# Performance work log

Hardware: AMD Instinct MI355X
Metric: run time of the kernel (lower is better)

The kernel has to match this reference:

```python
import jax, jax.numpy as jnp
import numpy as np

N = 10000      # num_nodes
RP = 16        # latent relations
E = 64         # emb_dim
R = 8000       # num triples (MLP input dim)
NT = 8000      # unique (s,o) pairs (unique by construction)
LW = 64        # lwidth
C = 16         # num_classes
NREL = 50      # num_rels (<= R columns actually used in nhots)


def setup_inputs() -> dict:
    rng = np.random.default_rng(0)
    # unique (s,o) pairs -> nt == R, deterministic shapes
    pair_ids = rng.choice(N * N, size=R, replace=False)
    s = (pair_ids // N).astype(np.int32)
    o = (pair_ids % N).astype(np.int32)
    p = rng.integers(0, NREL, size=R)
    nhots = np.zeros((NT, R), np.float32)
    nhots[np.arange(NT), p] = 1.0
    # replicate index construction from __init__ exactly
    rm = np.arange(RP, dtype=np.int32)[:, None]           # (RP,1)
    s_exp = np.broadcast_to(s[None, :], (RP, NT)).reshape(-1)
    o_exp = np.broadcast_to(o[None, :], (RP, NT)).reshape(-1)
    se = (s[None, :] * rm).reshape(-1)
    oe = (o[None, :] * rm).reshape(-1)
    hindices = np.stack([s_exp, oe], axis=1).astype(np.int32)  # into (N, N*RP)
    vindices = np.stack([se, o_exp], axis=1).astype(np.int32)  # into (N*RP, N)

    key = jax.random.key(0)
    ks = jax.random.split(key, 6)
    inv = lambda d: 1.0 / np.sqrt(d)
    return {
        'nhots': jnp.asarray(nhots),
        'w1a': jax.random.normal(ks[0], (R, LW), jnp.float32) * inv(R),
        'b1a': jnp.zeros((LW,), jnp.float32),
        'w1b': jax.random.normal(ks[1], (LW, RP), jnp.float32) * inv(LW),
        'b1b': jnp.zeros((RP,), jnp.float32),
        'w2a': jax.random.normal(ks[2], (R, LW), jnp.float32) * inv(R),
        'b2a': jnp.zeros((LW,), jnp.float32),
        'w2b': jax.random.normal(ks[3], (LW, RP), jnp.float32) * inv(LW),
        'b2b': jnp.zeros((RP,), jnp.float32),
        'weights1': jax.random.normal(ks[4], (RP, N, E), jnp.float32) * 0.02,
        'bias1': jnp.zeros((E,), jnp.float32),
        'weights2': jax.random.normal(ks[5], (RP, E, C), jnp.float32) * 0.02,
        'bias2': jnp.zeros((C,), jnp.float32),
        'hindices': jnp.asarray(hindices),
        'vindices': jnp.asarray(vindices),
    }


def _latents(nhots, wa, ba, wb, bb):
    # Linear -> ReLU -> Linear -> softmax over rp, then .t().reshape(-1)
    lat = jax.nn.softmax(jax.nn.relu(nhots @ wa + ba) @ wb + bb, axis=1)  # (NT, RP)
    return lat.T.reshape(-1)  # (RP*NT,) — rm-major, matching index construction


def reference(nhots, w1a, b1a, w1b, b1b, w2a, b2a, w2b, b2b,
              weights1, bias1, weights2, bias2, hindices, vindices):
    hrow, hcol = hindices[:, 0], hindices[:, 1]
    vrow, vcol = vindices[:, 0], vindices[:, 1]

    # --- layer 1: A1 (N, N*RP), column-normalized ---
    lat1 = _latents(nhots, w1a, b1a, w1b, b1b)
    colsum = jax.ops.segment_sum(lat1, hcol, num_segments=N * RP)
    lat1 = lat1 / colsum[hcol]
    Xw = weights1.reshape(RP * N, E)
    h = jax.ops.segment_sum(lat1[:, None] * Xw[hcol], hrow, num_segments=N)  # (N, E)
    h = jax.nn.relu(h + bias1)

    # --- layer 2: A2 (N*RP, N), row-normalized ---
    lat2 = _latents(nhots, w2a, b2a, w2b, b2b)
    rowsum = jax.ops.segment_sum(lat2, vrow, num_segments=N * RP)
    lat2 = lat2 / rowsum[vrow]
    h2 = jax.ops.segment_sum(lat2[:, None] * h[vcol], vrow, num_segments=N * RP)
    h2 = h2.reshape(RP, N, E)

    out = jnp.einsum('rhc,rnh->nc', weights2, h2) + bias2  # (N, C)
    return out
```

## Files before the change

### kernel.cpp

```cpp
#include <hip/hip_runtime.h>
#include <hip/hip_bf16.h>


#define N_     10000
#define RP_    16
#define E_     64
#define R_     8000
#define NT_    8000
#define C_     16
#define NE_    128000
#define BK_    32

#define WS_ZERO_UNITS 330080

__global__ void k_lat(const float* __restrict__ nhots,
                      const float* __restrict__ w1a, const float* __restrict__ b1a,
                      const float* __restrict__ w1b, const float* __restrict__ b1b,
                      const float* __restrict__ w2a, const float* __restrict__ b2a,
                      const float* __restrict__ w2b, const float* __restrict__ b2b,
                      const int* __restrict__ hind, const int* __restrict__ vind,
                      float* __restrict__ lat1t, float* __restrict__ lat2,
                      float* __restrict__ colsum, float* __restrict__ rowsum,
                      int* __restrict__ cnt, int* __restrict__ order2,
                      float* __restrict__ out, const float* __restrict__ bias2) {
    __shared__ float zb[4][128];
    __shared__ float r0[2];
    const int lane = threadIdx.x & 63;
    const int wv   = threadIdx.x >> 6;
    const int t    = blockIdx.x * 4 + wv;

    if (threadIdx.x < 80) {
        const int i = blockIdx.x * 80 + threadIdx.x;
        out[i] = bias2[i & 15];
    }

    const float4 v = reinterpret_cast<const float4*>(nhots + (size_t)t * R_)[lane];
    float acc1 = 0.f, acc2 = 0.f;
    const float comp[4] = {v.x, v.y, v.z, v.w};
    #pragma unroll
    for (int c = 0; c < 4; ++c) {
        unsigned long long m = __ballot(comp[c] != 0.0f);
        while (m) {
            const int src = __ffsll(m) - 1;
            m &= m - 1;
            const float val = __shfl(comp[c], src);
            const int col = src * 4 + c;
            acc1 += val * w1a[col * 64 + lane];
            acc2 += val * w2a[col * 64 + lane];
        }
    }
    if (threadIdx.x == 0) { r0[0] = 0.f; r0[1] = 0.f; }
    zb[wv][lane]      = fmaxf(acc1 + b1a[lane], 0.f);
    zb[wv][64 + lane] = fmaxf(acc2 + b2a[lane], 0.f);
    __syncthreads();

    const int g = lane >> 4, r = lane & 15;
    float pre = 0.f;
    if (g < 2) {
        const float* wb = (g == 0) ? w1b : w2b;
        pre = ((g == 0) ? b1b : b2b)[r];
        const float* z = &zb[wv][g * 64];
        #pragma unroll
        for (int l = 0; l < 64; ++l) pre += z[l] * wb[l * 16 + r];
    }
    float mx = pre;
    #pragma unroll
    for (int m = 8; m >= 1; m >>= 1) mx = fmaxf(mx, __shfl_xor(mx, m, 16));
    const float e = expf(pre - mx);
    float s = e;
    #pragma unroll
    for (int m = 8; m >= 1; m >>= 1) s += __shfl_xor(s, m, 16);
    const float lt = e / s;

    const int s_t = hind[2 * t];
    const int o_t = vind[2 * t + 1];
    if (g == 0) {
        lat1t[t * 16 + r] = lt;
        if (r) atomicAdd(colsum + o_t * r, lt);
        else   atomicAdd(&r0[0], lt);
    } else if (g == 1) {
        lat2[r * NT_ + t] = lt;
        if (r) atomicAdd(rowsum + s_t * r, lt);
        else   atomicAdd(&r0[1], lt);
    } else if (g == 2 && r == 0) {
        const int pos = atomicAdd(cnt + s_t, 1);
        order2[s_t * BK_ + pos] = t | (o_t << 13);
    }
    __syncthreads();
    if (threadIdx.x == 0) atomicAdd(colsum, r0[0]);
    if (threadIdx.x == 1) atomicAdd(rowsum, r0[1]);
}

__global__ void k_hg(const float* __restrict__ lat1t, const float* __restrict__ colsum,
                     const int* __restrict__ cnt, const int* __restrict__ order2,
                     const float* __restrict__ w1,
                     const float* __restrict__ bias1, float* __restrict__ hbuf) {
    const int lane = threadIdx.x & 63;
    const int n = blockIdx.x * 4 + (threadIdx.x >> 6);
    const int m = cnt[n];
    float acc = 0.f;
    for (int j = 0; j < m; ++j) {
        const int e = order2[n * BK_ + j];
        const int t   = e & 8191;
        const int o_t = e >> 13;
        float ln = 0.f;
        if (lane < 16) ln = lat1t[t * 16 + lane] / colsum[o_t * lane];
        #pragma unroll
        for (int r = 0; r < 16; ++r) {
            const float a = __shfl(ln, r);
            acc += a * w1[(o_t * r) * 64 + lane];
        }
    }
    hbuf[n * 64 + lane] = fmaxf(acc + bias1[lane], 0.f);
}

__global__ void k_h2all(const float* __restrict__ lat2, const float* __restrict__ rowsum,
                        const int* __restrict__ vind, const float* __restrict__ hbuf,
                        const float* __restrict__ w2, float* __restrict__ out,
                        float* __restrict__ h2r0, int* __restrict__ done) {
    const int lane = threadIdx.x & 63;
    const int wv   = threadIdx.x >> 6;

    if (blockIdx.x >= 512) {
        __shared__ int is_last;
        const int wg = (blockIdx.x - 512) * 4 + wv;
        float acc = 0.f;
        for (int t = wg; t < NT_; t += 256) {
            const int vc = vind[2 * t + 1];
            acc += lat2[t] * hbuf[vc * 64 + lane];
        }
        acc /= rowsum[0];
        atomicAdd(&h2r0[lane], acc);
        __threadfence();
        __syncthreads();
        if (threadIdx.x == 0) is_last = (atomicAdd(done, 1) == 63);
        __syncthreads();
        if (is_last) {
            __threadfence();
            if (threadIdx.x < 16) {
                const int c = threadIdx.x;
                float acc2 = 0.f;
                #pragma unroll
                for (int hh = 0; hh < 64; ++hh) acc2 += w2[hh * 16 + c] * h2r0[hh];
                atomicAdd(&out[c], acc2);
            }
        }
        return;
    }

    __shared__ float sw2[16384];
    for (int i = threadIdx.x; i < 16384; i += 256) sw2[i] = w2[i];
    __syncthreads();

    const int c = lane & 15;
    const int quarter = lane >> 4;
    for (int e = blockIdx.x * 4 + wv; e < 120000; e += 512 * 4) {
        const int k  = NT_ + e;
        const int q  = vind[2 * k];
        const int vc = vind[2 * k + 1];
        const float val = lat2[k] / rowsum[q];
        const int rp = q / N_;
        const int np = q - rp * N_;
        const float u = val * hbuf[vc * 64 + lane];
        float partial = 0.f;
        #pragma unroll
        for (int j = 0; j < 16; ++j) {
            const int hh = quarter * 16 + ((j + quarter) & 15);
            const float hv = __shfl(u, hh);
            partial += hv * sw2[rp * 1024 + hh * 16 + c];
        }
        partial += __shfl_xor(partial, 16);
        partial += __shfl_xor(partial, 32);
        if (quarter == 0) atomicAdd(&out[np * 16 + c], partial);
    }
}

extern "C" void kernel_launch(void* const* d_in, const int* in_sizes, int n_in,
                              void* d_out, int out_size, void* d_ws, size_t ws_size,
                              hipStream_t stream) {
    const float* nhots    = (const float*)d_in[0];
    const float* w1a      = (const float*)d_in[1];
    const float* b1a      = (const float*)d_in[2];
    const float* w1b      = (const float*)d_in[3];
    const float* b1b      = (const float*)d_in[4];
    const float* w2a      = (const float*)d_in[5];
    const float* b2a      = (const float*)d_in[6];
    const float* w2b      = (const float*)d_in[7];
    const float* b2b      = (const float*)d_in[8];
    const float* weights1 = (const float*)d_in[9];
    const float* bias1    = (const float*)d_in[10];
    const float* weights2 = (const float*)d_in[11];
    const float* bias2    = (const float*)d_in[12];
    const int*   hind     = (const int*)d_in[13];
    const int*   vind     = (const int*)d_in[14];
    float* out = (float*)d_out;

    float* ws     = (float*)d_ws;
    float* colsum = ws;
    float* rowsum = ws + 160000;
    float* h2r0   = ws + 320000;
    int*   cnt    = (int*)(ws + 320064);
    int*   done   = (int*)(ws + 330064);
    int*   order2 = (int*)(ws + 330080);
    float* hbuf   = ws + 650080;
    float* lat1t  = ws + 1290080;
    float* lat2   = ws + 1418080;

    hipMemsetAsync(d_ws, 0, WS_ZERO_UNITS * sizeof(float), stream);
    k_lat<<<2000, 256, 0, stream>>>(nhots, w1a, b1a, w1b, b1b, w2a, b2a, w2b, b2b,
                                    hind, vind, lat1t, lat2, colsum, rowsum, cnt,
                                    order2, out, bias2);
    k_hg<<<2500, 256, 0, stream>>>(lat1t, colsum, cnt, order2, weights1, bias1, hbuf);
    k_h2all<<<576, 256, 0, stream>>>(lat2, rowsum, vind, hbuf, weights2, out, h2r0, done);
}
```

Baseline: 454.9 us.

## Precompute h·W2 per node and replace scatter atomics with bucketed gather

```diff
diff --git a/kernel.cpp b/kernel.cpp
--- a/kernel.cpp
+++ b/kernel.cpp
@@ -8,10 +8,10 @@
 #define R_     8000
 #define NT_    8000
 #define C_     16
-#define NE_    128000
 #define BK_    32
-
-#define WS_ZERO_UNITS 330080
+#define BK2_   96
+
+#define WS_ZERO_UNITS 340000
 
 __global__ void k_lat(const float* __restrict__ nhots,
                       const float* __restrict__ w1a, const float* __restrict__ b1a,
@@ -22,17 +22,12 @@
                       float* __restrict__ lat1t, float* __restrict__ lat2,
                       float* __restrict__ colsum, float* __restrict__ rowsum,
                       int* __restrict__ cnt, int* __restrict__ order2,
-                      float* __restrict__ out, const float* __restrict__ bias2) {
+                      int* __restrict__ cnt2, int* __restrict__ bucket2) {
     __shared__ float zb[4][128];
     __shared__ float r0[2];
     const int lane = threadIdx.x & 63;
     const int wv   = threadIdx.x >> 6;
     const int t    = blockIdx.x * 4 + wv;
-
-    if (threadIdx.x < 80) {
-        const int i = blockIdx.x * 80 + threadIdx.x;
-        out[i] = bias2[i & 15];
-    }
 
     const float4 v = reinterpret_cast<const float4*>(nhots + (size_t)t * R_)[lane];
     float acc1 = 0.f, acc2 = 0.f;
@@ -82,96 +77,121 @@
         lat2[r * NT_ + t] = lt;
         if (r) atomicAdd(rowsum + s_t * r, lt);
         else   atomicAdd(&r0[1], lt);
-    } else if (g == 2 && r == 0) {
-        const int pos = atomicAdd(cnt + s_t, 1);
-        order2[s_t * BK_ + pos] = t | (o_t << 13);
+    } else if (g == 2) {
+        if (r == 0) {
+            const int pos = atomicAdd(cnt + s_t, 1);
+            order2[s_t * BK_ + pos] = t | (o_t << 13);
+        } else {
+            const int q = s_t * r;
+            const int rp = q / N_;
+            const int np = q - rp * N_;
+            const int pos = atomicAdd(cnt2 + np, 1);
+            bucket2[np * BK2_ + pos] = t | (r << 13) | (rp << 17);
+        }
     }
     __syncthreads();
     if (threadIdx.x == 0) atomicAdd(colsum, r0[0]);
     if (threadIdx.x == 1) atomicAdd(rowsum, r0[1]);
 }
 
-__global__ void k_hg(const float* __restrict__ lat1t, const float* __restrict__ colsum,
-                     const int* __restrict__ cnt, const int* __restrict__ order2,
-                     const float* __restrict__ w1,
-                     const float* __restrict__ bias1, float* __restrict__ hbuf) {
-    const int lane = threadIdx.x & 63;
-    const int n = blockIdx.x * 4 + (threadIdx.x >> 6);
-    const int m = cnt[n];
-    float acc = 0.f;
-    for (int j = 0; j < m; ++j) {
-        const int e = order2[n * BK_ + j];
-        const int t   = e & 8191;
-        const int o_t = e >> 13;
-        float ln = 0.f;
-        if (lane < 16) ln = lat1t[t * 16 + lane] / colsum[o_t * lane];
-        #pragma unroll
-        for (int r = 0; r < 16; ++r) {
-            const float a = __shfl(ln, r);
-            acc += a * w1[(o_t * r) * 64 + lane];
-        }
-    }
-    hbuf[n * 64 + lane] = fmaxf(acc + bias1[lane], 0.f);
-}
-
-__global__ void k_h2all(const float* __restrict__ lat2, const float* __restrict__ rowsum,
-                        const int* __restrict__ vind, const float* __restrict__ hbuf,
-                        const float* __restrict__ w2, float* __restrict__ out,
-                        float* __restrict__ h2r0, int* __restrict__ done) {
+__global__ void k_hgg(const float* __restrict__ lat1t, const float* __restrict__ colsum,
+                      const int* __restrict__ cnt, const int* __restrict__ order2,
+                      const float* __restrict__ w1, const float* __restrict__ bias1,
+                      const float* __restrict__ w2, float* __restrict__ g,
+                      float* __restrict__ out) {
+    __shared__ float sw2[16384];
     const int lane = threadIdx.x & 63;
     const int wv   = threadIdx.x >> 6;
-
-    if (blockIdx.x >= 512) {
-        __shared__ int is_last;
-        const int wg = (blockIdx.x - 512) * 4 + wv;
-        float acc = 0.f;
-        for (int t = wg; t < NT_; t += 256) {
-            const int vc = vind[2 * t + 1];
-            acc += lat2[t] * hbuf[vc * 64 + lane];
-        }
-        acc /= rowsum[0];
-        atomicAdd(&h2r0[lane], acc);
-        __threadfence();
-        __syncthreads();
-        if (threadIdx.x == 0) is_last = (atomicAdd(done, 1) == 63);
-        __syncthreads();
-        if (is_last) {
-            __threadfence();
-            if (threadIdx.x < 16) {
-                const int c = threadIdx.x;
-                float acc2 = 0.f;
-                #pragma unroll
-                for (int hh = 0; hh < 64; ++hh) acc2 += w2[hh * 16 + c] * h2r0[hh];
-                atomicAdd(&out[c], acc2);
-            }
-        }
-        return;
-    }
-
-    __shared__ float sw2[16384];
+    if (blockIdx.x == 0 && threadIdx.x < 16) out[threadIdx.x] = 0.f;
     for (int i = threadIdx.x; i < 16384; i += 256) sw2[i] = w2[i];
     __syncthreads();
 
-    const int c = lane & 15;
-    const int quarter = lane >> 4;
-    for (int e = blockIdx.x * 4 + wv; e < 120000; e += 512 * 4) {
-        const int k  = NT_ + e;
-        const int q  = vind[2 * k];
-        const int vc = vind[2 * k + 1];
-        const float val = lat2[k] / rowsum[q];
-        const int rp = q / N_;
-        const int np = q - rp * N_;
-        const float u = val * hbuf[vc * 64 + lane];
-        float partial = 0.f;
-        #pragma unroll
-        for (int j = 0; j < 16; ++j) {
-            const int hh = quarter * 16 + ((j + quarter) & 15);
-            const float hv = __shfl(u, hh);
-            partial += hv * sw2[rp * 1024 + hh * 16 + c];
-        }
-        partial += __shfl_xor(partial, 16);
-        partial += __shfl_xor(partial, 32);
-        if (quarter == 0) atomicAdd(&out[np * 16 + c], partial);
+    const int q = lane >> 4, c = lane & 15;
+    const int nbase = blockIdx.x * 32 + wv * 8;
+    float u[8];
+    #pragma unroll 1
+    for (int i = 0; i < 8; ++i) {
+        const int n = nbase + i;
+        float acc = 0.f;
+        if (n < N_) {
+            const int m = cnt[n];
+            for (int j = 0; j < m; ++j) {
+                const int e = order2[n * BK_ + j];
+                const int t = e & 8191, o_t = e >> 13;
+                float ln = 0.f;
+                if (lane < 16) ln = lat1t[t * 16 + lane] / colsum[o_t * lane];
+                #pragma unroll
+                for (int r = 0; r < 16; ++r)
+                    acc += __shfl(ln, r) * w1[(o_t * r) * 64 + lane];
+            }
+            acc = fmaxf(acc + bias1[lane], 0.f);
+        }
+        u[i] = acc;
+    }
+    float a[8][4];
+    #pragma unroll
+    for (int i = 0; i < 8; ++i)
+        #pragma unroll
+        for (int k = 0; k < 4; ++k) a[i][k] = 0.f;
+    for (int j = 0; j < 64; ++j) {
+        const int hh = (j + q) & 63;
+        float w4[4];
+        #pragma unroll
+        for (int k = 0; k < 4; ++k)
+            w4[k] = sw2[(q * 4 + k) * 1024 + hh * 16 + c];
+        #pragma unroll
+        for (int i = 0; i < 8; ++i) {
+            const float uh = __shfl(u[i], hh);
+            #pragma unroll
+            for (int k = 0; k < 4; ++k) a[i][k] += uh * w4[k];
+        }
+    }
+    #pragma unroll 1
+    for (int i = 0; i < 8; ++i) {
+        const int n = nbase + i;
+        if (n >= N_) break;
+        #pragma unroll
+        for (int k = 0; k < 4; ++k)
+            g[n * 256 + (q * 4 + k) * 16 + c] = a[i][k];
+    }
+}
+
+__global__ void k_gather(const float* __restrict__ lat2, const float* __restrict__ rowsum,
+                         const int* __restrict__ vind, const int* __restrict__ cnt2,
+                         const int* __restrict__ bucket2, const float* __restrict__ g,
+                         const float* __restrict__ bias2, float* __restrict__ out) {
+    const int lane = threadIdx.x & 63;
+    const int wv   = threadIdx.x >> 6;
+    const int q = lane >> 4, c = lane & 15;
+
+    if (blockIdx.x < 4) {
+        const int w = blockIdx.x * 4 + wv;
+        float acc = 0.f;
+        for (int t = w * 500 + q; t < (w + 1) * 500; t += 4) {
+            const int o_t = vind[2 * t + 1];
+            acc += lat2[t] * g[o_t * 256 + c];
+        }
+        acc += __shfl_xor(acc, 16);
+        acc += __shfl_xor(acc, 32);
+        if (q == 0) atomicAdd(&out[c], acc / rowsum[0]);
+        return;
+    }
+
+    const int np = (blockIdx.x - 4) * 4 + wv;
+    const int m2 = cnt2[np];
+    float acc = 0.f;
+    for (int j = q; j < m2; j += 4) {
+        const int e = bucket2[np * BK2_ + j];
+        const int t = e & 8191, r = (e >> 13) & 15, rp = (e >> 17) & 15;
+        const float val = lat2[r * NT_ + t] / rowsum[rp * N_ + np];
+        const int vc = vind[2 * t + 1];
+        acc += val * g[vc * 256 + rp * 16 + c];
+    }
+    acc += __shfl_xor(acc, 16);
+    acc += __shfl_xor(acc, 32);
+    if (q == 0) {
+        if (np == 0) atomicAdd(&out[c], acc + bias2[c]);
+        else         out[np * 16 + c] = acc + bias2[c];
     }
 }
 
@@ -195,21 +215,23 @@
     const int*   vind     = (const int*)d_in[14];
     float* out = (float*)d_out;
 
-    float* ws     = (float*)d_ws;
-    float* colsum = ws;
-    float* rowsum = ws + 160000;
-    float* h2r0   = ws + 320000;
-    int*   cnt    = (int*)(ws + 320064);
-    int*   done   = (int*)(ws + 330064);
-    int*   order2 = (int*)(ws + 330080);
-    float* hbuf   = ws + 650080;
-    float* lat1t  = ws + 1290080;
-    float* lat2   = ws + 1418080;
+    float* ws      = (float*)d_ws;
+    float* colsum  = ws;
+    float* rowsum  = ws + 160000;
+    int*   cnt     = (int*)(ws + 320000);
+    int*   cnt2    = (int*)(ws + 330000);
+    int*   order2  = (int*)(ws + 340000);
+    int*   bucket2 = (int*)(ws + 660000);
+    float* lat1t   = ws + 1620000;
+    float* lat2    = ws + 1748000;
+    float* gtab    = ws + 1876000;
 
     hipMemsetAsync(d_ws, 0, WS_ZERO_UNITS * sizeof(float), stream);
     k_lat<<<2000, 256, 0, stream>>>(nhots, w1a, b1a, w1b, b1b, w2a, b2a, w2b, b2b,
-                                    hind, vind, lat1t, lat2, colsum, rowsum, cnt,
-                                    order2, out, bias2);
-    k_hg<<<2500, 256, 0, stream>>>(lat1t, colsum, cnt, order2, weights1, bias1, hbuf);
-    k_h2all<<<576, 256, 0, stream>>>(lat2, rowsum, vind, hbuf, weights2, out, h2r0, done);
-}
+                                    hind, vind, lat1t, lat2, colsum, rowsum,
+                                    cnt, order2, cnt2, bucket2);
+    k_hgg<<<313, 256, 0, stream>>>(lat1t, colsum, cnt, order2, weights1, bias1,
+                                   weights2, gtab, out);
+    k_gather<<<2504, 256, 0, stream>>>(lat2, rowsum, vind, cnt2, bucket2, gtab,
+                                       bias2, out);
+}
```

Result: no change. 462.1 us (+1.6%).
